# Kernel optimization log

Hardware: AMD Instinct MI355X
Metric: run time of the kernel (lower is better)

## Reference

```python
import jax, jax.numpy as jnp
import numpy as np

V, E, D, L, B, EX = 50000, 128, 256, 400, 64, 200


def setup_inputs() -> dict:
    key = jax.random.key(0)
    ks = jax.random.split(key, 32)
    u = lambda k, shp, s=0.02: jax.random.uniform(k, shp, jnp.float32, -s, s)
    inp = {
        'input': jax.random.randint(ks[0], (B, 1), 0, V),
        'hidden_h': jax.random.normal(ks[1], (2, B, D), jnp.float32),
        'hidden_c': jax.random.normal(ks[2], (2, B, D), jnp.float32),
        'encoder_output': jax.random.normal(ks[3], (B, L, 2 * D), jnp.float32),
        'previous_context': jax.random.normal(ks[4], (B, 1, 2 * D), jnp.float32),
        'extended_input': jax.random.randint(ks[5], (B, L), 0, V + EX),
        'coverage': jax.random.uniform(ks[6], (B, L), jnp.float32),
        'padding_mask': jnp.ones((B, L), jnp.float32),
        'ex_size': EX,
        'output_step': 0,
        # parameters
        'emb_w': jax.random.normal(ks[7], (V, E), jnp.float32) * 1e-4,
        'lin_w': u(ks[8], (D, E + 2 * D)), 'lin_b': jnp.zeros((D,), jnp.float32),
        'w_ih': u(ks[9], (4 * D, D)), 'w_hh': u(ks[10], (4 * D, D)),
        'b_ih': jnp.zeros((4 * D,), jnp.float32).at[D:2 * D].set(1.0),
        'b_hh': jnp.zeros((4 * D,), jnp.float32),
        'red_h_w': u(ks[11], (D, 2 * D)), 'red_h_b': jnp.zeros((D,), jnp.float32),
        'red_c_w': u(ks[12], (D, 2 * D)), 'red_c_b': jnp.zeros((D,), jnp.float32),
        'wq_w': u(ks[13], (D, 2 * D)), 'wq_b': jnp.zeros((D,), jnp.float32),
        'cov_w': u(ks[14], (2 * D, 1)), 'cov_b': jnp.zeros((2 * D,), jnp.float32),
        'wk_w': u(ks[15], (D, 2 * D)), 'wk_b': jnp.zeros((D,), jnp.float32),
        'pre_w': u(ks[16], (D, 3 * D)), 'pre_b': jnp.zeros((D,), jnp.float32),
        'gen_w': u(ks[17], (V, D)), 'gen_b': jnp.zeros((V,), jnp.float32),
        'pgen_w': u(ks[18], (1, 5 * D)), 'pgen_b': jnp.zeros((1,), jnp.float32),
    }
    return inp


def reference(input, hidden_h, hidden_c, encoder_output, previous_context,
              extended_input, coverage, padding_mask, ex_size, output_step,
              emb_w, lin_w, lin_b, w_ih, w_hh, b_ih, b_hh,
              red_h_w, red_h_b, red_c_w, red_c_b,
              wq_w, wq_b, cov_w, cov_b, wk_w, wk_b,
              pre_w, pre_b, gen_w, gen_b, pgen_w, pgen_b):
    b = encoder_output.shape[0]
    d = w_ih.shape[1]
    scale = jnp.sqrt(jnp.float32(d))

    emb = emb_w[input[:, 0]][:, None, :]                      # [B,1,E]
    combine = jnp.concatenate([emb, previous_context], 2)     # [B,1,E+2D]
    x = combine @ lin_w.T + lin_b                             # [B,1,D]

    if output_step == 0:  # reduce bidirectional encoder state [2,B,D] -> [1,B,D]
        hs = jnp.transpose(hidden_h, (1, 0, 2)).reshape(b, 2 * d)
        cs = jnp.transpose(hidden_c, (1, 0, 2)).reshape(b, 2 * d)
        h = jax.nn.relu(hs @ red_h_w.T + red_h_b)
        c = jax.nn.relu(cs @ red_c_w.T + red_c_b)
    else:
        h, c = hidden_h[0], hidden_c[0]

    # single LSTM step (PyTorch gate order i,f,g,o)
    gates = x[:, 0] @ w_ih.T + b_ih + h @ w_hh.T + b_hh       # [B,4D]
    i, f, g, o = jnp.split(gates, 4, axis=1)
    c_new = jax.nn.sigmoid(f) * c + jax.nn.sigmoid(i) * jnp.tanh(g)
    h_new = jax.nn.sigmoid(o) * jnp.tanh(c_new)
    lstm_out = h_new[:, None, :]                              # [B,1,D]

    # scaled-dot coverage attention
    query = jnp.concatenate([h_new, c_new], 1)                # [B,2D]
    Q = jnp.tanh(query @ wq_w.T + wq_b)                       # [B,D]
    word_feature = encoder_output + (coverage[..., None] @ cov_w.T + cov_b)
    K = jnp.tanh(word_feature @ wk_w.T + wk_b)                # [B,L,D]
    score = jnp.einsum('bd,bld->bl', Q / scale, K)
    score = jnp.where(padding_mask > 0, score, jnp.float32(-1e18))
    attention = jax.nn.softmax(score, axis=1)                 # [B,L]
    weighted_context = jnp.einsum('bl,bld->bd', attention, encoder_output)[:, None, :]

    p_gen = jax.nn.sigmoid(
        jnp.concatenate([x[:, 0], weighted_context[:, 0], h_new, c_new], 1)
        @ pgen_w.T + pgen_b)                                  # [B,1]

    owc = jnp.concatenate([weighted_context, lstm_out], 2)[:, 0]  # [B,3D]
    pregen = owc @ pre_w.T + pre_b                            # [B,D]
    vocab_dist = p_gen * jax.nn.softmax(pregen @ gen_w.T + gen_b, axis=1)
    att_dist = (1.0 - p_gen) * attention                      # [B,L]

    vocab_ext = jnp.concatenate(
        [vocab_dist, jnp.zeros((b, ex_size), vocab_dist.dtype)], 1)
    final_dist = vocab_ext.at[jnp.arange(b)[:, None], extended_input].add(att_dist)

    hidden = (h_new[None], c_new[None])
    return (final_dist, hidden, weighted_context, attention, coverage, p_gen)
```

## Files before the change

kernel.cpp:

```cpp
#include <hip/hip_runtime.h>
#include <math.h>

#define BB 64
#define DD 256
#define LL 400
#define VV 50000
#define EE 128
#define NB 782

typedef __attribute__((ext_vector_type(8))) short short8v;
typedef __attribute__((ext_vector_type(4))) short short4v;
typedef __attribute__((ext_vector_type(4))) float f32x4;

__device__ __forceinline__ float sigmoidf_(float x){ return 1.0f/(1.0f+expf(-x)); }

__device__ __forceinline__ short f2bf(float f){
    unsigned u = __builtin_bit_cast(unsigned, f);
    u += 0x7fffu + ((u>>16)&1u);
    return (short)(u>>16);
}

#define ROW_X   0
#define ROW_WC  256
#define ROW_H   768
#define ROW_C   1024

#define DOT8(col, wptr, kk, acc) { \
    float a0_=(col)[((kk)+0)*64], a1_=(col)[((kk)+1)*64], a2_=(col)[((kk)+2)*64], a3_=(col)[((kk)+3)*64], \
          a4_=(col)[((kk)+4)*64], a5_=(col)[((kk)+5)*64], a6_=(col)[((kk)+6)*64], a7_=(col)[((kk)+7)*64]; \
    asm volatile("" : "+v"(a0_),"+v"(a1_),"+v"(a2_),"+v"(a3_),"+v"(a4_),"+v"(a5_),"+v"(a6_),"+v"(a7_)); \
    acc += a0_*(wptr)[(kk)+0] + a1_*(wptr)[(kk)+1] + a2_*(wptr)[(kk)+2] + a3_*(wptr)[(kk)+3] \
         + a4_*(wptr)[(kk)+4] + a5_*(wptr)[(kk)+5] + a6_*(wptr)[(kk)+6] + a7_*(wptr)[(kk)+7]; }

__device__ __forceinline__ float dot4v(f32x4 a, f32x4 b){
    return a[0]*b[0] + a[1]*b[1] + a[2]*b[2] + a[3]*b[3];
}

__global__ __launch_bounds__(256) void k_front1(
    const int* __restrict__ inp, const float* __restrict__ hh, const float* __restrict__ hc,
    const float* __restrict__ prev, const float* __restrict__ emb_w,
    const float* __restrict__ lin_w, const float* __restrict__ lin_b,
    const float* __restrict__ rhw, const float* __restrict__ rhb,
    const float* __restrict__ rcw, const float* __restrict__ rcb,
    const int* __restrict__ step_p,
    const float* __restrict__ wk_w, const float* __restrict__ wk_b,
    const float* __restrict__ cov_w, const float* __restrict__ cov_b,
    float* __restrict__ actT, float* __restrict__ WhT, float* __restrict__ WcT0,
    short* __restrict__ Wb, float* __restrict__ u, float* __restrict__ v2,
    float* __restrict__ o_wc)
{
    const int d = blockIdx.x, y = blockIdx.y, t = threadIdx.x;
    const int b = t >> 2, kq = t & 3;
    __shared__ float lw[640];
    __shared__ float red[256];

    if (y == 3){
        if (t < 128) o_wc[d*128 + t] = 0.f;
        const float* row = wk_w + (size_t)d*512;
        float su=0.f, sv=0.f;
        for (int j=t; j<512; j+=256){
            float wv = row[j];
            Wb[(size_t)(j>>3)*2048 + d*8 + (j&7)] = f2bf(wv);
            su += wv*cov_w[j];
            sv += wv*cov_b[j];
        }
        float* rs = lw;
        float* rv = red;
        rs[t]=su; rv[t]=sv; __syncthreads();
        for (int s=128;s>0;s>>=1){ if(t<s){rs[t]+=rs[t+s]; rv[t]+=rv[t+s];} __syncthreads(); }
        if (t==0){ u[d]=rs[0]; v2[d]=rv[0] + wk_b[d]; }
        return;
    }

    if (y == 0){
        if (t < 160) ((f32x4*)lw)[t] = ((const f32x4*)(lin_w + (size_t)d*640))[t];
        __syncthreads();
        const f32x4* lw4 = (const f32x4*)lw;
        const f32x4* er4 = (const f32x4*)(emb_w + (size_t)inp[b]*EE);
        const f32x4* pv4 = (const f32x4*)(prev + (size_t)b*512);
        float acc = 0.f;
        for (int i=kq; i<160; i+=16){
            f32x4 v0 = (i    < 32) ? er4[i]    : pv4[i-32];
            f32x4 v1 = (i+4  < 32) ? er4[i+4]  : pv4[i-28];
            f32x4 v2_ = pv4[i-24];
            f32x4 v3 = pv4[i-20];
            if (i+8  < 32) v2_ = er4[i+8];
            if (i+12 < 32) v3 = er4[i+12];
            asm volatile("" : "+v"(v0),"+v"(v1),"+v"(v2_),"+v"(v3));
            acc += dot4v(v0, lw4[i]) + dot4v(v1, lw4[i+4])
                 + dot4v(v2_, lw4[i+8]) + dot4v(v3, lw4[i+12]);
        }
        acc += __shfl_xor(acc,1); acc += __shfl_xor(acc,2);
        if (kq == 0) actT[(ROW_X + d)*64 + b] = lin_b[d] + acc;
        return;
    }

    const float* src  = (y==1) ? hh  : hc;
    float*       dstT = (y==1) ? WhT : WcT0;
    if (*step_p == 0){
        const float* wrow = ((y==1) ? rhw : rcw) + (size_t)d*512;
        const float  bias = ((y==1) ? rhb : rcb)[d];
        if (t < 128) ((f32x4*)lw)[t] = ((const f32x4*)wrow)[t];
        __syncthreads();
        const f32x4* lw4 = (const f32x4*)lw;
        const f32x4* s0 = (const f32x4*)(src + (size_t)b*DD);
        const f32x4* s1 = (const f32x4*)(src + (size_t)BB*DD + (size_t)b*DD);
        float acc = 0.f;
        for (int i=kq; i<128; i+=16){
            f32x4 v0 = (i    < 64) ? s0[i]    : s1[i-64];
            f32x4 v1 = (i+4  < 64) ? s0[i+4]  : s1[i-60];
            f32x4 v2_ = (i+8 < 64) ? s0[i+8]  : s1[i-56];
            f32x4 v3 = (i+12 < 64) ? s0[i+12] : s1[i-52];
            asm volatile("" : "+v"(v0),"+v"(v1),"+v"(v2_),"+v"(v3));
            acc += dot4v(v0, lw4[i]) + dot4v(v1, lw4[i+4])
                 + dot4v(v2_, lw4[i+8]) + dot4v(v3, lw4[i+12]);
        }
        acc += __shfl_xor(acc,1); acc += __shfl_xor(acc,2);
        if (kq == 0){
            float a = bias + acc;
            dstT[d*64 + b] = a>0.f ? a : 0.f;
        }
    } else {
        if (t < 64) dstT[d*64 + t] = src[(size_t)t*DD + d];
    }
}

__global__ __launch_bounds__(256) void k_gl(
    const float* __restrict__ actT, const float* __restrict__ WhT, const float* __restrict__ WcT0,
    const float* __restrict__ w_ih, const float* __restrict__ w_hh,
    const float* __restrict__ b_ih, const float* __restrict__ b_hh,
    float* __restrict__ o_h, float* __restrict__ o_c, float* __restrict__ actT_out)
{
    const int d = blockIdx.x, t = threadIdx.x;
    const int b = t & 63, gi = t >> 6;
    __shared__ float wih[4][256];
    __shared__ float whh[4][256];
    __shared__ float gl[4][64];

    const int gr = gi*DD + d;
    ((f32x4*)&wih[gi][0])[b] = ((const f32x4*)(w_ih + (size_t)gr*DD))[b];
    ((f32x4*)&whh[gi][0])[b] = ((const f32x4*)(w_hh + (size_t)gr*DD))[b];
    __syncthreads();

    const float* xcol = actT + ROW_X*64 + b;
    const float* hcol = WhT + b;
    float a0=0.f, a1=0.f;
    for (int kk=0; kk<256; kk+=8){
        DOT8(xcol, &wih[gi][0], kk, a0);
        DOT8(hcol, &whh[gi][0], kk, a1);
    }
    gl[gi][b] = a0 + a1 + b_ih[gr] + b_hh[gr];
    __syncthreads();

    if (t < 64){
        float iv = sigmoidf_(gl[0][t]);
        float fv = sigmoidf_(gl[1][t]);
        float gv = tanhf(gl[2][t]);
        float ov = sigmoidf_(gl[3][t]);
        float cn = fv*WcT0[d*64 + t] + iv*gv;
        float hn = ov*tanhf(cn);
        o_c[(size_t)t*DD + d] = cn;
        o_h[(size_t)t*DD + d] = hn;
        actT_out[(ROW_C + d)*64 + t] = cn;
        actT_out[(ROW_H + d)*64 + t] = hn;
    }
}

__global__ __launch_bounds__(256) void k_q2(
    const float* __restrict__ actT,
    const float* __restrict__ wq_w, const float* __restrict__ wq_b,
    float* __restrict__ Qs)
{
    const int d = blockIdx.x, t = threadIdx.x;
    const int b = t & 63, w = t >> 6;
    __shared__ float lw[512];
    __shared__ float red[4][64];
    if (t < 128) ((f32x4*)lw)[t] = ((const f32x4*)(wq_w + (size_t)d*512))[t];
    __syncthreads();
    const float* col = actT + ROW_H*64 + b;
    float acc = 0.f;
    const int k0 = w*128;
    for (int kk=k0; kk<k0+128; kk+=8)
        DOT8(col, lw, kk, acc);
    red[w][b] = acc; __syncthreads();
    if (t < 64)
        Qs[(size_t)t*DD + d] = tanhf(wq_b[d] + red[0][t]+red[1][t]+red[2][t]+red[3][t]) * 0.0625f;
}

#define SC_MFMA(KS, BF) \
  { const int cc_ = (KS)*4 + qw; \
    short8v a0_ = *(const short8v*)&As[lr*512 + ((cc_ ^ (lr&7))<<3)]; \
    short8v a1_ = *(const short8v*)&As[(16+lr)*512 + ((cc_ ^ (lr&7))<<3)]; \
    acc0 = __builtin_amdgcn_mfma_f32_16x16x32_bf16(a0_, BF, acc0, 0,0,0); \
    acc1 = __builtin_amdgcn_mfma_f32_16x16x32_bf16(a1_, BF, acc1, 0,0,0); }

#define SC_CHUNK(KC, B0,B1,B2,B3) \
    SC_MFMA((KC)*4+0, B0); SC_MFMA((KC)*4+1, B1); \
    SC_MFMA((KC)*4+2, B2); SC_MFMA((KC)*4+3, B3);

__global__ __launch_bounds__(1024, 4) void k_score_mfma(
    const float* __restrict__ enc, const short* __restrict__ Wb,
    const float* __restrict__ u, const float* __restrict__ v2,
    const float* __restrict__ Qs, const float* __restrict__ cov,
    const float* __restrict__ pmask, float* __restrict__ score)
{
    const int b  = blockIdx.y;
    const int l0 = blockIdx.x * 32;
    const int tid = threadIdx.x;
    const int wave = tid >> 6, lane = tid & 63;
    const int qw = lane >> 4, lr = lane & 15;
    const int col = wave*16 + lr;

    __shared__ __align__(16) short As[32*512];
    __shared__ float Red[16][32];

    const short* bp = Wb + (size_t)qw*2048 + col*8;
    short8v c0 = *(const short8v*)(bp +  0*8192);
    short8v c1 = *(const short8v*)(bp +  1*8192);
    short8v c2 = *(const short8v*)(bp +  2*8192);
    short8v c3 = *(const short8v*)(bp +  3*8192);

    const int arow = tid >> 5;
    const int af   = tid & 31;
    const bool aval = (l0 + arow) < LL;
    const float4* aptr = (const float4*)(enc + ((size_t)(b*LL + (aval ? l0+arow : 0)))*512);
    float4 areg[4];
    #pragma unroll
    for (int j=0; j<4; j++)
        areg[j] = aval ? aptr[af + j*32] : float4{0.f,0.f,0.f,0.f};

    #pragma unroll
    for (int j=0; j<4; j++){
        const int fi   = af + j*32;
        const int c    = fi >> 1;
        const int half = fi & 1;
        const int cs   = c ^ (arow & 7);
        short4v t4;
        t4[0]=f2bf(areg[j].x); t4[1]=f2bf(areg[j].y);
        t4[2]=f2bf(areg[j].z); t4[3]=f2bf(areg[j].w);
        *(short4v*)&As[arow*512 + cs*8 + half*4] = t4;
    }
    __syncthreads();

    f32x4 acc0 = f32x4{0.f,0.f,0.f,0.f};
    f32x4 acc1 = f32x4{0.f,0.f,0.f,0.f};

    short8v n0 = *(const short8v*)(bp +  4*8192);
    short8v n1 = *(const short8v*)(bp +  5*8192);
    short8v n2 = *(const short8v*)(bp +  6*8192);
    short8v n3 = *(const short8v*)(bp +  7*8192);
    SC_CHUNK(0, c0,c1,c2,c3);
    asm volatile("" : "+v"(n0),"+v"(n1),"+v"(n2),"+v"(n3));

    c0 = *(const short8v*)(bp +  8*8192);
    c1 = *(const short8v*)(bp +  9*8192);
    c2 = *(const short8v*)(bp + 10*8192);
    c3 = *(const short8v*)(bp + 11*8192);
    SC_CHUNK(1, n0,n1,n2,n3);
    asm volatile("" : "+v"(c0),"+v"(c1),"+v"(c2),"+v"(c3));

    n0 = *(const short8v*)(bp + 12*8192);
    n1 = *(const short8v*)(bp + 13*8192);
    n2 = *(const short8v*)(bp + 14*8192);
    n3 = *(const short8v*)(bp + 15*8192);
    SC_CHUNK(2, c0,c1,c2,c3);
    asm volatile("" : "+v"(n0),"+v"(n1),"+v"(n2),"+v"(n3));

    SC_CHUNK(3, n0,n1,n2,n3);

    const float qv = Qs[b*DD + col];
    const float uv = u[col];
    const float vv = v2[col];
    #pragma unroll
    for (int rf=0; rf<2; rf++){
        const f32x4 acc = rf ? acc1 : acc0;
        const int rbase = l0 + rf*16 + qw*4;
        float cv[4];
        if (rbase < LL){
            float4 c4v = *(const float4*)(cov + (size_t)b*LL + rbase);
            cv[0]=c4v.x; cv[1]=c4v.y; cv[2]=c4v.z; cv[3]=c4v.w;
        } else { cv[0]=cv[1]=cv[2]=cv[3]=0.f; }
        #pragma unroll
        for (int r=0; r<4; r++){
            float s = qv * tanhf(acc[r] + cv[r]*uv + vv);
            s += __shfl_xor(s,1); s += __shfl_xor(s,2);
            s += __shfl_xor(s,4); s += __shfl_xor(s,8);
            if (lr == 0) Red[wave][rf*16 + qw*4 + r] = s;
        }
    }
    __syncthreads();
    if (tid < 32){
        int l = l0 + tid;
        if (l < LL){
            float s = 0.f;
            #pragma unroll
            for (int w2=0; w2<16; w2++) s += Red[w2][tid];
            score[b*LL + l] = (pmask[b*LL+l] > 0.f) ? s : -1e18f;
        }
    }
}

__global__ __launch_bounds__(512) void k_wcsm(
    const float* __restrict__ score, const float* __restrict__ cov_in,
    const float* __restrict__ enc,
    float* __restrict__ attn_out, float* __restrict__ cov_out, float* __restrict__ wc)
{
    const int b = blockIdx.y, ch = blockIdx.x;
    const int t = threadIdx.x;
    __shared__ float sc[LL];
    __shared__ float red[512];

    float v = (t < LL) ? score[b*LL + t] : -INFINITY;
    red[t] = v; __syncthreads();
    for (int s=256;s>0;s>>=1){ if(t<s) red[t]=fmaxf(red[t],red[t+s]); __syncthreads(); }
    float m = red[0]; __syncthreads();
    float e = (t < LL) ? expf(v - m) : 0.f;
    if (t < LL) sc[t] = e;
    red[t] = e; __syncthreads();
    for (int s=256;s>0;s>>=1){ if(t<s) red[t]+=red[t+s]; __syncthreads(); }
    const float inv = 1.0f / red[0];

    const int l0 = ch * (LL/16);
    float s = 0.f;
    #pragma unroll 5
    for (int l=l0; l<l0+LL/16; ++l)
        s += sc[l] * enc[((size_t)(b*LL+l))*512 + t];
    atomicAdd(&wc[b*512 + t], s * inv);

    if (ch == 0 && t < LL){
        attn_out[b*LL + t] = sc[t] * inv;
        cov_out[b*LL + t]  = cov_in[b*LL + t];
    }
}

__global__ __launch_bounds__(256) void k_tr(const float* __restrict__ wc,
                                            float* __restrict__ actT)
{
    const int j0 = blockIdx.x * 64;
    __shared__ float tile[64][65];
    const int t = threadIdx.x;
    const int c = t & 63, r0 = t >> 6;
    #pragma unroll
    for (int bb = r0; bb < 64; bb += 4)
        tile[bb][c] = wc[(size_t)bb*512 + j0 + c];
    __syncthreads();
    #pragma unroll
    for (int jj = r0; jj < 64; jj += 4)
        actT[(ROW_WC + j0 + jj)*64 + c] = tile[c][jj];
}

__global__ __launch_bounds__(256) void k_pregen(
    const float* __restrict__ actT,
    const float* __restrict__ pre_w, const float* __restrict__ pre_b,
    const float* __restrict__ pgen_w, const float* __restrict__ pgen_b,
    short* __restrict__ pregenb, float* __restrict__ pgen_out)
{
    const int d = blockIdx.x, t = threadIdx.x;
    const int b = t & 63, w = t >> 6;
    __shared__ float pw[768];
    __shared__ float red[4][64];
    if (t < 192) ((f32x4*)pw)[t] = ((const f32x4*)(pre_w + (size_t)d*768))[t];
    __syncthreads();
    const float* col = actT + ROW_WC*64 + b;
    float acc = 0.f;
    const int k0 = w*192;
    for (int kk=k0; kk<k0+192; kk+=8)
        DOT8(col, pw, kk, acc);
    red[w][b] = acc; __syncthreads();
    if (t < 64)
        pregenb[(size_t)t*DD + d] = f2bf(pre_b[d] + red[0][t]+red[1][t]+red[2][t]+red[3][t]);

    if (blockIdx.x == 0){
        __syncthreads();
        const float* colx = actT + b;
        float p = 0.f;
        const int j0 = w*320;
        for (int jj=j0; jj<j0+320; jj+=8)
            DOT8(colx, pgen_w, jj, p);
        red[w][b] = p; __syncthreads();
        if (t < 64)
            pgen_out[t] = sigmoidf_(red[0][t]+red[1][t]+red[2][t]+red[3][t] + pgen_b[0]);
    }
}

#define GEN_SLICE(KS, RA, RB) \
  { short8v bb_; \
    bb_[0]=f2bf(RA[0]); bb_[1]=f2bf(RA[1]); bb_[2]=f2bf(RA[2]); bb_[3]=f2bf(RA[3]); \
    bb_[4]=f2bf(RB[0]); bb_[5]=f2bf(RB[1]); bb_[6]=f2bf(RB[2]); bb_[7]=f2bf(RB[3]); \
    const int cc_ = (KS)*4 + qw; \
    const int cs_ = (cc_ ^ (lr&7))<<3; \
    short8v aa0_ = *(const short8v*)&As[(lr     )*256 + cs_]; \
    short8v aa1_ = *(const short8v*)&As[(16+lr)*256 + cs_]; \
    short8v aa2_ = *(const short8v*)&As[(32+lr)*256 + cs_]; \
    short8v aa3_ = *(const short8v*)&As[(48+lr)*256 + cs_]; \
    acc0 = __builtin_amdgcn_mfma_f32_16x16x32_bf16(aa0_, bb_, acc0, 0,0,0); \
    acc1 = __builtin_amdgcn_mfma_f32_16x16x32_bf16(aa1_, bb_, acc1, 0,0,0); \
    acc2 = __builtin_amdgcn_mfma_f32_16x16x32_bf16(aa2_, bb_, acc2, 0,0,0); \
    acc3 = __builtin_amdgcn_mfma_f32_16x16x32_bf16(aa3_, bb_, acc3, 0,0,0); }

__global__ __launch_bounds__(256, 3) void k_gen_mfma(
    const short* __restrict__ pregenb, const float* __restrict__ gen_w,
    const float* __restrict__ gen_b, float* __restrict__ logits,
    float* __restrict__ blkM, float* __restrict__ blkS, int W)
{
    const int blk = blockIdx.x;
    const int v0 = blk * 64;
    const int tid = threadIdx.x;
    const int wave = tid>>6, lane = tid&63, qw = lane>>4, lr = lane&15;

    __shared__ __align__(16) short As[64*256];
    __shared__ float pm[4][64];
    __shared__ float ps[4][64];

    const int vrow = v0 + wave*16 + lr;
    const bool bval = (vrow < VV);
    const f32x4* bq = (const f32x4*)(gen_w + (size_t)(bval ? vrow : 0)*DD + qw*8);
    f32x4 a0 = bq[ 0], a1 = bq[ 1];
    f32x4 a2 = bq[ 8], a3 = bq[ 9];
    f32x4 a4 = bq[16], a5 = bq[17];
    f32x4 a6 = bq[24], a7 = bq[25];

    #pragma unroll
    for (int j=0; j<8; j++){
        int f = tid + j*256;
        int row = f >> 5, c = f & 31;
        short8v s = ((const short8v*)pregenb)[f];
        *(short8v*)&As[row*256 + ((c ^ (row&7))<<3)] = s;
    }
    __syncthreads();

    f32x4 acc0 = f32x4{0.f,0.f,0.f,0.f};
    f32x4 acc1 = f32x4{0.f,0.f,0.f,0.f};
    f32x4 acc2 = f32x4{0.f,0.f,0.f,0.f};
    f32x4 acc3 = f32x4{0.f,0.f,0.f,0.f};

    f32x4 b0 = bq[32], b1 = bq[33];
    f32x4 b2 = bq[40], b3 = bq[41];
    f32x4 b4 = bq[48], b5 = bq[49];
    f32x4 b6 = bq[56], b7 = bq[57];

    GEN_SLICE(0, a0, a1);
    GEN_SLICE(1, a2, a3);
    GEN_SLICE(2, a4, a5);
    GEN_SLICE(3, a6, a7);
    asm volatile("" : "+v"(b0),"+v"(b1),"+v"(b2),"+v"(b3),
                      "+v"(b4),"+v"(b5),"+v"(b6),"+v"(b7));
    GEN_SLICE(4, b0, b1);
    GEN_SLICE(5, b2, b3);
    GEN_SLICE(6, b4, b5);
    GEN_SLICE(7, b6, b7);

    f32x4 accs[4] = {acc0, acc1, acc2, acc3};
    const int v = v0 + wave*16 + lr;
    const bool vv = (v < VV);
    const float gb = vv ? gen_b[v] : 0.f;
    #pragma unroll
    for (int rf=0; rf<4; rf++){
        #pragma unroll
        for (int r=0; r<4; r++){
            float lg = accs[rf][r] + gb;
            int bt = rf*16 + qw*4 + r;
            if (vv) logits[(size_t)bt*W + v] = lg;
            float x = vv ? lg : -1e30f;
            float mx = x;
            mx = fmaxf(mx, __shfl_xor(mx,1));
            mx = fmaxf(mx, __shfl_xor(mx,2));
            mx = fmaxf(mx, __shfl_xor(mx,4));
            mx = fmaxf(mx, __shfl_xor(mx,8));
            float e = vv ? expf(x - mx) : 0.f;
            e += __shfl_xor(e,1); e += __shfl_xor(e,2);
            e += __shfl_xor(e,4); e += __shfl_xor(e,8);
            if (lr == 0){ pm[wave][bt] = mx; ps[wave][bt] = e; }
        }
    }
    __syncthreads();
    if (tid < 64){
        float M = fmaxf(fmaxf(pm[0][tid], pm[1][tid]), fmaxf(pm[2][tid], pm[3][tid]));
        float S = ps[0][tid]*expf(pm[0][tid]-M) + ps[1][tid]*expf(pm[1][tid]-M)
                + ps[2][tid]*expf(pm[2][tid]-M) + ps[3][tid]*expf(pm[3][tid]-M);
        blkM[(size_t)tid*NB + blk] = M;
        blkS[(size_t)tid*NB + blk] = S;
    }
}

__global__ __launch_bounds__(256) void k_vred(
    const float* __restrict__ blkM, const float* __restrict__ blkS,
    float* __restrict__ Ms, float* __restrict__ Ss)
{
    const int b = blockIdx.x, t = threadIdx.x;
    __shared__ float red[256];
    float m = -INFINITY;
    for (int i=t; i<NB; i+=256) m = fmaxf(m, blkM[(size_t)b*NB + i]);
    red[t]=m; __syncthreads();
    for (int s=128;s>0;s>>=1){ if(t<s) red[t]=fmaxf(red[t],red[t+s]); __syncthreads(); }
    const float M = red[0]; __syncthreads();
    float s = 0.f;
    for (int i=t; i<NB; i+=256) s += blkS[(size_t)b*NB + i] * expf(blkM[(size_t)b*NB + i] - M);
    red[t]=s; __syncthreads();
    for (int st=128;st>0;st>>=1){ if(t<st) red[t]+=red[t+st]; __syncthreads(); }
    if (t==0){ Ms[b]=M; Ss[b]=red[0]; }
}

__global__ void k_final(float* __restrict__ out, const float* __restrict__ Ms,
                        const float* __restrict__ Ss, const float* __restrict__ pgen, int W)
{
    size_t idx = (size_t)blockIdx.x*blockDim.x + threadIdx.x;
    if (idx >= (size_t)BB*W) return;
    int b = (int)(idx / W);
    int v = (int)(idx % W);
    float* row = out + (size_t)b*W;
    if (v < VV) row[v] = pgen[b] * expf(row[v]-Ms[b]) / Ss[b];
    else        row[v] = 0.f;
}

__global__ void k_scatter(float* __restrict__ out, const int* __restrict__ ext,
                          const float* __restrict__ attn, const float* __restrict__ pgen, int W)
{
    int idx = blockIdx.x*blockDim.x + threadIdx.x;
    if (idx >= BB*LL) return;
    int b = idx / LL;
    atomicAdd(out + (size_t)b*W + ext[idx], (1.0f - pgen[b]) * attn[idx]);
}

extern "C" void kernel_launch(void* const* d_in, const int* in_sizes, int n_in,
                              void* d_out, int out_size, void* d_ws, size_t ws_size,
                              hipStream_t stream)
{
    const int*   inp     = (const int*)  d_in[0];
    const float* hh      = (const float*)d_in[1];
    const float* hc      = (const float*)d_in[2];
    const float* enc     = (const float*)d_in[3];
    const float* prev    = (const float*)d_in[4];
    const int*   ext     = (const int*)  d_in[5];
    const float* cov     = (const float*)d_in[6];
    const float* pmask   = (const float*)d_in[7];
    const int*   step_p  = (const int*)  d_in[9];
    const float* emb_w   = (const float*)d_in[10];
    const float* lin_w   = (const float*)d_in[11];
    const float* lin_b   = (const float*)d_in[12];
    const float* w_ih    = (const float*)d_in[13];
    const float* w_hh    = (const float*)d_in[14];
    const float* b_ih    = (const float*)d_in[15];
    const float* b_hh    = (const float*)d_in[16];
    const float* rhw     = (const float*)d_in[17];
    const float* rhb     = (const float*)d_in[18];
    const float* rcw     = (const float*)d_in[19];
    const float* rcb     = (const float*)d_in[20];
    const float* wq_w    = (const float*)d_in[21];
    const float* wq_b    = (const float*)d_in[22];
    const float* cov_w   = (const float*)d_in[23];
    const float* cov_b   = (const float*)d_in[24];
    const float* wk_w    = (const float*)d_in[25];
    const float* wk_b    = (const float*)d_in[26];
    const float* pre_w   = (const float*)d_in[27];
    const float* pre_b   = (const float*)d_in[28];
    const float* gen_w   = (const float*)d_in[29];
    const float* gen_b   = (const float*)d_in[30];
    const float* pgen_w  = (const float*)d_in[31];
    const float* pgen_b  = (const float*)d_in[32];

    const int W = out_size / BB - 4*DD - 2*LL - 1;
    float* out     = (float*)d_out;
    float* o_final = out;
    float* o_h     = out + (size_t)BB*W;
    float* o_c     = o_h + BB*DD;
    float* o_wc    = o_c + BB*DD;
    float* o_attn  = o_wc + BB*2*DD;
    float* o_cov   = o_attn + BB*LL;
    float* o_pgen  = o_cov + BB*LL;

    float* W_actT   = (float*)d_ws;
    float* W_whT    = W_actT + 1280*64;
    float* W_wcT0   = W_whT + BB*DD;
    float* W_q      = W_wcT0 + BB*DD;
    float* W_score  = W_q + BB*DD;
    float* W_m      = W_score + BB*LL;
    float* W_s      = W_m + BB;
    float* W_u      = W_s + BB;
    float* W_v2     = W_u + DD;
    float* W_blkM   = W_v2 + DD;
    float* W_blkS   = W_blkM + (size_t)BB*NB;
    short* W_wb     = (short*)(W_blkS + (size_t)BB*NB);
    short* W_pgb    = (short*)(W_wb + 64*2048);

    k_front1<<<dim3(DD,4), 256, 0, stream>>>(inp, hh, hc, prev, emb_w, lin_w, lin_b,
                                             rhw, rhb, rcw, rcb, step_p,
                                             wk_w, wk_b, cov_w, cov_b,
                                             W_actT, W_whT, W_wcT0, W_wb, W_u, W_v2, o_wc);
    k_gl<<<DD, 256, 0, stream>>>(W_actT, W_whT, W_wcT0, w_ih, w_hh, b_ih, b_hh,
                                 o_h, o_c, W_actT);
    k_q2<<<DD, 256, 0, stream>>>(W_actT, wq_w, wq_b, W_q);
    k_score_mfma<<<dim3(13, BB), 1024, 0, stream>>>(enc, W_wb, W_u, W_v2, W_q, cov, pmask, W_score);
    k_wcsm<<<dim3(16, BB), 512, 0, stream>>>(W_score, cov, enc, o_attn, o_cov, o_wc);
    k_tr<<<8, 256, 0, stream>>>(o_wc, W_actT);
    k_pregen<<<DD, 256, 0, stream>>>(W_actT, pre_w, pre_b, pgen_w, pgen_b, W_pgb, o_pgen);
    k_gen_mfma<<<NB, 256, 0, stream>>>(W_pgb, gen_w, gen_b, o_final, W_blkM, W_blkS, W);
    k_vred<<<BB, 256, 0, stream>>>(W_blkM, W_blkS, W_m, W_s);
    k_final<<<(int)(((size_t)BB*W+255)/256), 256, 0, stream>>>(o_final, W_m, W_s, o_pgen, W);
    k_scatter<<<(BB*LL+255)/256, 256, 0, stream>>>(o_final, ext, o_attn, o_pgen, W);
}
```

Baseline: 138.3 us.

## Fuse attention softmax and context into score kernel; store logits as bf16

Measured after the change: 132.4 us. 1.04x faster.

```diff
diff --git a/kernel.cpp b/kernel.cpp
--- a/kernel.cpp
+++ b/kernel.cpp
@@ -18,6 +18,10 @@
     unsigned u = __builtin_bit_cast(unsigned, f);
     u += 0x7fffu + ((u>>16)&1u);
     return (short)(u>>16);
+}
+__device__ __forceinline__ float bf2f(unsigned short b){
+    unsigned u = ((unsigned)b) << 16;
+    return __builtin_bit_cast(float, u);
 }
 
 #define ROW_X   0
@@ -47,7 +51,7 @@
     const float* __restrict__ cov_w, const float* __restrict__ cov_b,
     float* __restrict__ actT, float* __restrict__ WhT, float* __restrict__ WcT0,
     short* __restrict__ Wb, float* __restrict__ u, float* __restrict__ v2,
-    float* __restrict__ o_wc)
+    float* __restrict__ wcpart, float* __restrict__ Ssum)
 {
     const int d = blockIdx.x, y = blockIdx.y, t = threadIdx.x;
     const int b = t >> 2, kq = t & 3;
@@ -55,7 +59,8 @@
     __shared__ float red[256];
 
     if (y == 3){
-        if (t < 128) o_wc[d*128 + t] = 0.f;
+        if (t < 128) wcpart[d*128 + t] = 0.f;
+        if (d == 0 && t >= 128 && t < 192) Ssum[t-128] = 0.f;
         const float* row = wk_w + (size_t)d*512;
         float su=0.f, sv=0.f;
         for (int j=t; j<512; j+=256){
@@ -202,7 +207,8 @@
     const float* __restrict__ enc, const short* __restrict__ Wb,
     const float* __restrict__ u, const float* __restrict__ v2,
     const float* __restrict__ Qs, const float* __restrict__ cov,
-    const float* __restrict__ pmask, float* __restrict__ score)
+    const float* __restrict__ pmask,
+    float* __restrict__ Ev, float* __restrict__ Ssum, float* __restrict__ wcpart)
 {
     const int b  = blockIdx.y;
     const int l0 = blockIdx.x * 32;
@@ -213,6 +219,7 @@
 
     __shared__ __align__(16) short As[32*512];
     __shared__ float Red[16][32];
+    __shared__ float esh[32];
 
     const short* bp = Wb + (size_t)qw*2048 + col*8;
     short8v c0 = *(const short8v*)(bp +  0*8192);
@@ -291,58 +298,66 @@
     __syncthreads();
     if (tid < 32){
         int l = l0 + tid;
+        float e = 0.f;
         if (l < LL){
             float s = 0.f;
             #pragma unroll
             for (int w2=0; w2<16; w2++) s += Red[w2][tid];
-            score[b*LL + l] = (pmask[b*LL+l] > 0.f) ? s : -1e18f;
-        }
-    }
-}
-
-__global__ __launch_bounds__(512) void k_wcsm(
-    const float* __restrict__ score, const float* __restrict__ cov_in,
-    const float* __restrict__ enc,
-    float* __restrict__ attn_out, float* __restrict__ cov_out, float* __restrict__ wc)
-{
-    const int b = blockIdx.y, ch = blockIdx.x;
-    const int t = threadIdx.x;
-    __shared__ float sc[LL];
-    __shared__ float red[512];
-
-    float v = (t < LL) ? score[b*LL + t] : -INFINITY;
-    red[t] = v; __syncthreads();
-    for (int s=256;s>0;s>>=1){ if(t<s) red[t]=fmaxf(red[t],red[t+s]); __syncthreads(); }
-    float m = red[0]; __syncthreads();
-    float e = (t < LL) ? expf(v - m) : 0.f;
-    if (t < LL) sc[t] = e;
-    red[t] = e; __syncthreads();
-    for (int s=256;s>0;s>>=1){ if(t<s) red[t]+=red[t+s]; __syncthreads(); }
-    const float inv = 1.0f / red[0];
-
-    const int l0 = ch * (LL/16);
-    float s = 0.f;
-    #pragma unroll 5
-    for (int l=l0; l<l0+LL/16; ++l)
-        s += sc[l] * enc[((size_t)(b*LL+l))*512 + t];
-    atomicAdd(&wc[b*512 + t], s * inv);
-
-    if (ch == 0 && t < LL){
-        attn_out[b*LL + t] = sc[t] * inv;
+            e = (pmask[b*LL+l] > 0.f) ? expf(s) : 0.f;
+            Ev[b*LL + l] = e;
+        }
+        esh[tid] = e;
+        float se = e;
+        se += __shfl_xor(se,1); se += __shfl_xor(se,2);
+        se += __shfl_xor(se,4); se += __shfl_xor(se,8);
+        se += __shfl_xor(se,16);
+        if (tid == 0) atomicAdd(&Ssum[b], se);
+    }
+    __syncthreads();
+    if (tid < 512){
+        const int c  = tid >> 3;
+        const int p  = tid & 7;
+        float acc = 0.f;
+        #pragma unroll
+        for (int l=0; l<32; l++){
+            unsigned short bits = (unsigned short)As[l*512 + ((c ^ (l&7))<<3) + p];
+            acc += esh[l] * bf2f(bits);
+        }
+        atomicAdd(&wcpart[b*512 + tid], acc);
+    }
+}
+
+__global__ __launch_bounds__(512) void k_attn(
+    const float* __restrict__ Ev, const float* __restrict__ Ssum,
+    const float* __restrict__ cov_in,
+    float* __restrict__ attn_out, float* __restrict__ cov_out)
+{
+    const int b = blockIdx.x, t = threadIdx.x;
+    if (t < LL){
+        const float inv = 1.0f / Ssum[b];
+        attn_out[b*LL + t] = Ev[b*LL + t] * inv;
         cov_out[b*LL + t]  = cov_in[b*LL + t];
     }
 }
 
-__global__ __launch_bounds__(256) void k_tr(const float* __restrict__ wc,
+__global__ __launch_bounds__(256) void k_tr(const float* __restrict__ wcpart,
+                                            const float* __restrict__ Ssum,
+                                            float* __restrict__ o_wc,
                                             float* __restrict__ actT)
 {
     const int j0 = blockIdx.x * 64;
     __shared__ float tile[64][65];
+    __shared__ float invs[64];
     const int t = threadIdx.x;
     const int c = t & 63, r0 = t >> 6;
+    if (t < 64) invs[t] = 1.0f / Ssum[t];
+    __syncthreads();
     #pragma unroll
-    for (int bb = r0; bb < 64; bb += 4)
-        tile[bb][c] = wc[(size_t)bb*512 + j0 + c];
+    for (int bb = r0; bb < 64; bb += 4){
+        float v = wcpart[(size_t)bb*512 + j0 + c] * invs[bb];
+        tile[bb][c] = v;
+        o_wc[(size_t)bb*512 + j0 + c] = v;
+    }
     __syncthreads();
     #pragma unroll
     for (int jj = r0; jj < 64; jj += 4)
@@ -400,8 +415,8 @@
 
 __global__ __launch_bounds__(256, 3) void k_gen_mfma(
     const short* __restrict__ pregenb, const float* __restrict__ gen_w,
-    const float* __restrict__ gen_b, float* __restrict__ logits,
-    float* __restrict__ blkM, float* __restrict__ blkS, int W)
+    const float* __restrict__ gen_b, short* __restrict__ lgb,
+    float* __restrict__ blkM, float* __restrict__ blkS)
 {
     const int blk = blockIdx.x;
     const int v0 = blk * 64;
@@ -460,7 +475,7 @@
         for (int r=0; r<4; r++){
             float lg = accs[rf][r] + gb;
             int bt = rf*16 + qw*4 + r;
-            if (vv) logits[(size_t)bt*W + v] = lg;
+            if (vv) lgb[(size_t)bt*VV + v] = f2bf(lg);
             float x = vv ? lg : -1e30f;
             float mx = x;
             mx = fmaxf(mx, __shfl_xor(mx,1));
@@ -501,16 +516,19 @@
     if (t==0){ Ms[b]=M; Ss[b]=red[0]; }
 }
 
-__global__ void k_final(float* __restrict__ out, const float* __restrict__ Ms,
-                        const float* __restrict__ Ss, const float* __restrict__ pgen, int W)
+__global__ void k_final(const short* __restrict__ lgb, float* __restrict__ out,
+                        const float* __restrict__ Ms, const float* __restrict__ Ss,
+                        const float* __restrict__ pgen, int W)
 {
     size_t idx = (size_t)blockIdx.x*blockDim.x + threadIdx.x;
     if (idx >= (size_t)BB*W) return;
     int b = (int)(idx / W);
     int v = (int)(idx % W);
     float* row = out + (size_t)b*W;
-    if (v < VV) row[v] = pgen[b] * expf(row[v]-Ms[b]) / Ss[b];
-    else        row[v] = 0.f;
+    if (v < VV){
+        float lg = bf2f((unsigned short)lgb[(size_t)b*VV + v]);
+        row[v] = pgen[b] * expf(lg - Ms[b]) / Ss[b];
+    } else row[v] = 0.f;
 }
 
 __global__ void k_scatter(float* __restrict__ out, const int* __restrict__ ext,
@@ -573,8 +591,10 @@
     float* W_whT    = W_actT + 1280*64;
     float* W_wcT0   = W_whT + BB*DD;
     float* W_q      = W_wcT0 + BB*DD;
-    float* W_score  = W_q + BB*DD;
-    float* W_m      = W_score + BB*LL;
+    float* W_e      = W_q + BB*DD;
+    float* W_S      = W_e + BB*LL;
+    float* W_wcp    = W_S + BB;
+    float* W_m      = W_wcp + BB*512;
     float* W_s      = W_m + BB;
     float* W_u      = W_s + BB;
     float* W_v2     = W_u + DD;
@@ -582,20 +602,23 @@
     float* W_blkS   = W_blkM + (size_t)BB*NB;
     short* W_wb     = (short*)(W_blkS + (size_t)BB*NB);
     short* W_pgb    = (short*)(W_wb + 64*2048);
+    short* W_lg     = W_pgb + BB*DD;
 
     k_front1<<<dim3(DD,4), 256, 0, stream>>>(inp, hh, hc, prev, emb_w, lin_w, lin_b,
                                              rhw, rhb, rcw, rcb, step_p,
                                              wk_w, wk_b, cov_w, cov_b,
-                                             W_actT, W_whT, W_wcT0, W_wb, W_u, W_v2, o_wc);
+                                             W_actT, W_whT, W_wcT0, W_wb, W_u, W_v2,
+                                             W_wcp, W_S);
     k_gl<<<DD, 256, 0, stream>>>(W_actT, W_whT, W_wcT0, w_ih, w_hh, b_ih, b_hh,
                                  o_h, o_c, W_actT);
     k_q2<<<DD, 256, 0, stream>>>(W_actT, wq_w, wq_b, W_q);
-    k_score_mfma<<<dim3(13, BB), 1024, 0, stream>>>(enc, W_wb, W_u, W_v2, W_q, cov, pmask, W_score);
-    k_wcsm<<<dim3(16, BB), 512, 0, stream>>>(W_score, cov, enc, o_attn, o_cov, o_wc);
-    k_tr<<<8, 256, 0, stream>>>(o_wc, W_actT);
+    k_score_mfma<<<dim3(13, BB), 1024, 0, stream>>>(enc, W_wb, W_u, W_v2, W_q, cov, pmask,
+                                                    W_e, W_S, W_wcp);
+    k_attn<<<BB, 512, 0, stream>>>(W_e, W_S, cov, o_attn, o_cov);
+    k_tr<<<8, 256, 0, stream>>>(W_wcp, W_S, o_wc, W_actT);
     k_pregen<<<DD, 256, 0, stream>>>(W_actT, pre_w, pre_b, pgen_w, pgen_b, W_pgb, o_pgen);
-    k_gen_mfma<<<NB, 256, 0, stream>>>(W_pgb, gen_w, gen_b, o_final, W_blkM, W_blkS, W);
+    k_gen_mfma<<<NB, 256, 0, stream>>>(W_pgb, gen_w, gen_b, W_lg, W_blkM, W_blkS);
     k_vred<<<BB, 256, 0, stream>>>(W_blkM, W_blkS, W_m, W_s);
-    k_final<<<(int)(((size_t)BB*W+255)/256), 256, 0, stream>>>(o_final, W_m, W_s, o_pgen, W);
+    k_final<<<(int)(((size_t)BB*W+255)/256), 256, 0, stream>>>(W_lg, o_final, W_m, W_s, o_pgen, W);
     k_scatter<<<(BB*LL+255)/256, 256, 0, stream>>>(o_final, ext, o_attn, o_pgen, W);
 }
```
